# Kernel optimization log

Hardware: AMD Instinct MI355X
Metric: run time of the kernel (lower is better)

The kernel has to match this reference:

```python
import jax, jax.numpy as jnp
import numpy as np
from functools import partial

DN = ('NCHW', 'OIHW', 'NCHW')

def _conv(x, w, b, stride, pad):
    y = jax.lax.conv_general_dilated(x, w, (stride, stride), [(pad, pad), (pad, pad)], dimension_numbers=DN)
    return y + b[None, :, None, None]

def _leaky(x, s):
    return jnp.where(x >= 0, x, s * x)

def _lstm_gates(pre, c):
    # PyTorch gate order: i, f, g, o
    i, f, g, o = jnp.split(pre, 4, axis=-1)
    c_new = jax.nn.sigmoid(f) * c + jax.nn.sigmoid(i) * jnp.tanh(g)
    h_new = jax.nn.sigmoid(o) * jnp.tanh(c_new)
    return h_new, c_new

def setup_inputs() -> dict:
    key = jax.random.key(0)
    ks = iter(jax.random.split(key, 32))
    s = 0.05
    d = {}
    d['x'] = jax.random.normal(next(ks), (128, 3, 64, 64), jnp.float32)
    # conv stack params
    d['w1'] = jax.random.normal(next(ks), (64, 3, 7, 7)) * s;   d['b1'] = jnp.zeros((64,))
    d['w2'] = jax.random.normal(next(ks), (128, 64, 7, 7)) * s; d['b2'] = jnp.zeros((128,))
    d['w3'] = jax.random.normal(next(ks), (256, 128, 5, 5)) * s; d['b3'] = jnp.zeros((256,))
    d['w4'] = jax.random.normal(next(ks), (512, 256, 5, 5)) * s; d['b4'] = jnp.zeros((512,))
    d['w5'] = jax.random.normal(next(ks), (512, 512, 5, 5)) * s; d['b5'] = jnp.zeros((512,))
    # 2-layer LSTM (hidden=512), PyTorch layout: W_ih [4H, In], W_hh [4H, H]
    H = 512
    for l in range(2):
        d[f'wih{l}'] = jax.random.normal(next(ks), (4 * H, H)) * s
        d[f'whh{l}'] = jax.random.normal(next(ks), (4 * H, H)) * s
        d[f'bih{l}'] = jnp.zeros((4 * H,))
        d[f'bhh{l}'] = jnp.zeros((4 * H,))
    # FC head
    d['fw1'] = jax.random.normal(next(ks), (512, 512)) * s; d['fb1'] = jnp.zeros((512,))
    d['fw2'] = jax.random.normal(next(ks), (13, 512)) * s;  d['fb2'] = jnp.zeros((13,))
    return d

TIMESTEPS = 20

def reference(x, w1, b1, w2, b2, w3, b3, w4, b4, w5, b5,
              wih0, whh0, bih0, bhh0, wih1, whh1, bih1, bhh1,
              fw1, fb1, fw2, fb2):
    B = x.shape[0]
    h = _conv(x, w1, b1, 2, 3); h = _leaky(h, 0.2)
    h = _conv(h, w2, b2, 2, 0); h = _leaky(h, 0.2)
    h = _conv(h, w3, b3, 1, 0); h = _leaky(h, 0.2)
    h = _conv(h, w4, b4, 1, 0); h = _leaky(h, 0.2)
    h = _conv(h, w5, b5, 1, 0); h = _leaky(h, 0.2)
    feat = h.reshape(B, -1)  # [B, 512]
    H = 512
    # input to layer-0 is constant across timesteps: precompute Wx once
    xW0 = feat @ wih0.T + bih0 + bhh0  # [B, 4H]
    zeros = jnp.zeros((B, H), feat.dtype)

    def step(carry, _):
        h0, c0, h1, c1 = carry
        h0n, c0n = _lstm_gates(xW0 + h0 @ whh0.T, c0)
        pre1 = h0n @ wih1.T + bih1 + bhh1 + h1 @ whh1.T
        h1n, c1n = _lstm_gates(pre1, c1)
        return (h0n, c0n, h1n, c1n), h1n

    _, ys = jax.lax.scan(step, (zeros, zeros, zeros, zeros), None, length=TIMESTEPS)
    y = ys.reshape(TIMESTEPS * B, H)
    y = _leaky(y @ fw1.T + fb1, 0.01)
    y = jax.nn.sigmoid(y @ fw2.T + fb2)
    return y
```

## Files before the change

### kernel.cpp

```cpp
#include <hip/hip_runtime.h>
#include <math.h>

typedef _Float16 half_t;
typedef __attribute__((ext_vector_type(8))) _Float16 f16x8;
typedef __attribute__((ext_vector_type(4))) _Float16 f16x4;
typedef __attribute__((ext_vector_type(4))) float f32x4;

#define LEAKY(v, s) ((v) >= 0.f ? (v) : (s) * (v))

__device__ __forceinline__ float sig_(float x) { return 1.f / (1.f + expf(-x)); }
__device__ __forceinline__ half_t f2h(float f) { return (half_t)f; }

#define GLD(gp, lp)                                              \
  __builtin_amdgcn_global_load_lds(                              \
      (const __attribute__((address_space(1))) void*)(gp),       \
      (__attribute__((address_space(3))) void*)(lp), 16, 0, 0)

#define PHASE_WAIT(N)                                            \
  asm volatile("s_waitcnt vmcnt(" #N ")" ::: "memory");          \
  __builtin_amdgcn_s_barrier();                                  \
  __builtin_amdgcn_sched_barrier(0)

#define QOFF0 2048LL
#define QOFF1 4096LL
#define QOFF2 135168LL
#define QOFF3 266240LL
#define QOFF4 5283840LL
#define QOFF5 5310464LL
#define QOFF6 6359040LL
#define QOFF7 6621184LL
#define QOFF8 7669760LL
#define QOFF9 9766912LL

__global__ void prep_all(
    const float* __restrict__ x, const float* __restrict__ w1,
    const float* __restrict__ wih0, const float* __restrict__ whh0,
    const float* __restrict__ bih0, const float* __restrict__ bhh0,
    const float* __restrict__ wih1, const float* __restrict__ whh1,
    const float* __restrict__ bih1, const float* __restrict__ bhh1,
    const float* __restrict__ fw1,
    float* __restrict__ bg0, float* __restrict__ bg1,
    float* __restrict__ czero, unsigned* __restrict__ hzero,
    half_t* __restrict__ xpad, half_t* __restrict__ w1r,
    half_t* __restrict__ wih0h, half_t* __restrict__ fw1h,
    half_t* __restrict__ wcat0h, half_t* __restrict__ wcat1h) {
  long long i = (long long)blockIdx.x * blockDim.x + threadIdx.x;
  if (i < QOFF0) {
    bg0[i] = bih0[i] + bhh0[i];
  } else if (i < QOFF1) {
    long long j = i - QOFF0;
    bg1[j] = bih1[j] + bhh1[j];
  } else if (i < QOFF2) {
    czero[i - QOFF1] = 0.f;
  } else if (i < QOFF3) {
    hzero[i - QOFF2] = 0u;
  } else if (i < QOFF4) {
    long long j = i - QOFF3;
    int c = j & 7;
    long long t = j >> 3;
    int iw = t % 70; t /= 70;
    int ih = t % 70;
    int n = t / 70;
    float v = 0.f;
    if (c < 3 && ih >= 3 && ih < 67 && iw >= 3 && iw < 67)
      v = x[((n * 3 + c) * 64 + (ih - 3)) * 64 + (iw - 3)];
    xpad[j] = f2h(v);
  } else if (i < QOFF5) {
    int j = (int)(i - QOFF4);
    int kg = j % 416, co = j / 416;
    int ci = kg & 7, tap = kg >> 3;
    float v = 0.f;
    if (tap < 49 && ci < 3) {
      int kh = tap / 7, kw = tap % 7;
      v = w1[((co * 3 + ci) * 7 + kh) * 7 + kw];
    }
    w1r[j] = f2h(v);
  } else if (i < QOFF6) {
    int j = (int)(i - QOFF5);
    wih0h[j] = f2h(wih0[j]);
  } else if (i < QOFF7) {
    int j = (int)(i - QOFF6);
    fw1h[j] = f2h(fw1[j]);
  } else if (i < QOFF8) {
    int j = (int)(i - QOFF7);
    int r = j >> 9, k = j & 511;
    int u = r >> 2, g = r & 3;
    wcat0h[j] = f2h(whh0[(g * 512 + u) * 512 + k]);
  } else if (i < QOFF9) {
    int j = (int)(i - QOFF8);
    int r = j >> 10, k = j & 1023;
    int u = r >> 2, g = r & 3;
    int row = g * 512 + u;
    wcat1h[j] = f2h(k < 512 ? wih1[row * 512 + k] : whh1[row * 512 + (k - 512)]);
  }
}

__global__ __launch_bounds__(256) void prep_wT(
    const float* __restrict__ w2, const float* __restrict__ w3,
    const float* __restrict__ w4, const float* __restrict__ w5,
    half_t* __restrict__ w2r, half_t* __restrict__ w3r,
    half_t* __restrict__ w4r, half_t* __restrict__ w5r) {
  __shared__ float T[12800];
  int bid = blockIdx.x, tid = threadIdx.x;
  const float* W;
  half_t* D;
  int co, Cin, TAP, lg2;
  if (bid < 128) {
    W = w2; D = w2r; co = bid; Cin = 64; TAP = 49; lg2 = 6;
  } else if (bid < 384) {
    W = w3; D = w3r; co = bid - 128; Cin = 128; TAP = 25; lg2 = 7;
  } else if (bid < 896) {
    W = w4; D = w4r; co = bid - 384; Cin = 256; TAP = 25; lg2 = 8;
  } else {
    W = w5; D = w5r; co = bid - 896; Cin = 512; TAP = 25; lg2 = 9;
  }
  int n = Cin * TAP;
  const float* src = W + (size_t)co * n;
  for (int i = tid; i < n; i += 256) T[i] = src[i];
  __syncthreads();
  half_t* dst = D + (size_t)co * n;
  for (int j = tid; j < n; j += 256) {
    int ci = j & (Cin - 1);
    int tap = j >> lg2;
    dst[j] = f2h(T[ci * TAP + tap]);
  }
}

template <int KW, int S, int LOG2CIN, int OUTMODE>
__global__ __launch_bounds__(256) void conv_mfma(
    const half_t* __restrict__ xin, const half_t* __restrict__ wr,
    const float* __restrict__ bias, void* __restrict__ outp,
    int Hin, int Win, int Hout, int Wout, int Cout, int K, int ktiles, float slope,
    long long zstride) {
  constexpr int CIN = 1 << LOG2CIN;
  __shared__ half_t lds[4][4096];
  const int tid = threadIdx.x;
  const int lane = tid & 63, wid = tid >> 6;
  const int sRow = tid >> 2, sCh = tid & 3;
  const int sSwz = sCh ^ ((sRow ^ (sRow >> 2)) & 3);
  const int kt0 = blockIdx.z * ktiles;
  const half_t* gArow = wr + (size_t)(blockIdx.y * 64 + sRow) * K + sSwz * 8;
  int p = blockIdx.x * 64 + sRow;
  int hw = Hout * Wout;
  int n = p / hw;
  int rem = p - n * hw;
  int oh = rem / Wout;
  int ow = rem - oh * Wout;
  const half_t* xb = xin + ((size_t)(n * Hin + oh * S) * Win + ow * S) * CIN;
  const int fr = lane & 15, fc = lane >> 4;
  const int r0 = (wid & 1) * 32, c0 = (wid >> 1) * 32;
  const int sw = (fc ^ ((fr ^ (fr >> 2)) & 3)) * 8;
  const int ia0 = (r0 + fr) * 32 + sw;
  const int ia1 = (r0 + 16 + fr) * 32 + sw;
  const int ib0 = 2048 + (c0 + fr) * 32 + sw;
  const int ib1 = 2048 + (c0 + 16 + fr) * 32 + sw;

  auto stage = [&](int t, int buf) {
    GLD(gArow + (size_t)(kt0 + t) * 32, &lds[buf][wid * 512]);
    int kg = (kt0 + t) * 32 + sSwz * 8;
    int ci = kg & (CIN - 1);
    int tap = kg >> LOG2CIN;
    int kh = tap / KW, kw = tap - kh * KW;
    GLD(xb + (kh * Win + kw) * CIN + ci, &lds[buf][2048 + wid * 512]);
  };

  f32x4 acc00 = {0.f, 0.f, 0.f, 0.f};
  f32x4 acc01 = acc00, acc10 = acc00, acc11 = acc00;

  auto compute = [&](int buf) {
    const half_t* L = &lds[buf][0];
    f16x8 a0 = *(const f16x8*)&L[ia0];
    f16x8 a1 = *(const f16x8*)&L[ia1];
    f16x8 b0 = *(const f16x8*)&L[ib0];
    f16x8 b1 = *(const f16x8*)&L[ib1];
    acc00 = __builtin_amdgcn_mfma_f32_16x16x32_f16(a0, b0, acc00, 0, 0, 0);
    acc01 = __builtin_amdgcn_mfma_f32_16x16x32_f16(a0, b1, acc01, 0, 0, 0);
    acc10 = __builtin_amdgcn_mfma_f32_16x16x32_f16(a1, b0, acc10, 0, 0, 0);
    acc11 = __builtin_amdgcn_mfma_f32_16x16x32_f16(a1, b1, acc11, 0, 0, 0);
  };

  stage(0, 0);
  stage(1, 1);
  stage(2, 2);
  int t = 0;
  for (; t < ktiles - 3; ++t) {
    PHASE_WAIT(4);
    stage(t + 3, (t + 3) & 3);
    compute(t & 3);
  }
  PHASE_WAIT(4);
  compute(t & 3);
  ++t;
  PHASE_WAIT(2);
  compute(t & 3);
  ++t;
  PHASE_WAIT(0);
  compute(t & 3);

#pragma unroll
  for (int am = 0; am < 2; ++am) {
#pragma unroll
    for (int bn = 0; bn < 2; ++bn) {
      f32x4 a = am == 0 ? (bn == 0 ? acc00 : acc01) : (bn == 0 ? acc10 : acc11);
      int co = blockIdx.y * 64 + r0 + am * 16 + fc * 4;
      int px = blockIdx.x * 64 + c0 + bn * 16 + fr;
      size_t o = (size_t)px * Cout + co;
      if (OUTMODE == 2) {
        float* pb = (float*)outp + (size_t)blockIdx.z * zstride;
        *(f32x4*)&pb[o] = a;
      } else {
        f32x4 bb = *(const f32x4*)&bias[co];
        f32x4 v;
#pragma unroll
        for (int j = 0; j < 4; ++j) {
          float tt = a[j] + bb[j];
          v[j] = LEAKY(tt, slope);
        }
        if (OUTMODE == 1) {
          *(f32x4*)&((float*)outp)[o] = v;
        } else {
          f16x4 hv;
#pragma unroll
          for (int j = 0; j < 4; ++j) hv[j] = f2h(v[j]);
          *(f16x4*)&((half_t*)outp)[o] = hv;
        }
      }
    }
  }
}

template <int KW, int S, int LOG2CIN, int OUTMODE>
__global__ __launch_bounds__(256) void conv_mfma128(
    const half_t* __restrict__ xin, const half_t* __restrict__ wr,
    const float* __restrict__ bias, void* __restrict__ outp,
    int Hin, int Win, int Hout, int Wout, int Cout, int K, int ktiles, float slope,
    long long zstride) {
  constexpr int CIN = 1 << LOG2CIN;
  __shared__ half_t lds[4][8192];
  const int tid = threadIdx.x;
  const int lane = tid & 63, wid = tid >> 6;
  const int sRow = tid >> 2, sCh = tid & 3;
  const int sSwz = sCh ^ ((sRow ^ (sRow >> 2)) & 3);
  const int kt0 = blockIdx.z * ktiles;
  const half_t* gA0 = wr + (size_t)(blockIdx.y * 128 + sRow) * K + sSwz * 8;
  const half_t* gA1 = wr + (size_t)(blockIdx.y * 128 + 64 + sRow) * K + sSwz * 8;
  int hw = Hout * Wout;
  int p0 = blockIdx.x * 128 + sRow;
  int n0 = p0 / hw, r0p = p0 - n0 * hw, oh0 = r0p / Wout, ow0 = r0p - oh0 * Wout;
  const half_t* xb0 = xin + ((size_t)(n0 * Hin + oh0 * S) * Win + ow0 * S) * CIN;
  int p1 = p0 + 64;
  int n1 = p1 / hw, r1p = p1 - n1 * hw, oh1 = r1p / Wout, ow1 = r1p - oh1 * Wout;
  const half_t* xb1 = xin + ((size_t)(n1 * Hin + oh1 * S) * Win + ow1 * S) * CIN;

  const int fr = lane & 15, fc = lane >> 4;
  const int wr_ = wid & 1, wc_ = wid >> 1;
  const int sw = (fc ^ ((fr ^ (fr >> 2)) & 3)) * 8;
  const int iaB = (wr_ * 64 + fr) * 32 + sw;
  const int ibB = 4096 + (wc_ * 64 + fr) * 32 + sw;

  auto stage = [&](int t, int buf) {
    half_t* LB = &lds[buf][0];
    GLD(gA0 + (size_t)(kt0 + t) * 32, LB + wid * 512);
    GLD(gA1 + (size_t)(kt0 + t) * 32, LB + 2048 + wid * 512);
    int kg = (kt0 + t) * 32 + sSwz * 8;
    int ci = kg & (CIN - 1);
    int tap = kg >> LOG2CIN;
    int kh = tap / KW, kw = tap - kh * KW;
    int xoff = (kh * Win + kw) * CIN + ci;
    GLD(xb0 + xoff, LB + 4096 + wid * 512);
    GLD(xb1 + xoff, LB + 6144 + wid * 512);
  };

  f32x4 acc[4][4];
#pragma unroll
  for (int i = 0; i < 4; ++i)
#pragma unroll
    for (int j = 0; j < 4; ++j) acc[i][j] = (f32x4){0.f, 0.f, 0.f, 0.f};

  auto compute = [&](int buf) {
    const half_t* L = &lds[buf][0];
    f16x8 a[4], b[4];
#pragma unroll
    for (int fi = 0; fi < 4; ++fi) a[fi] = *(const f16x8*)&L[iaB + fi * 512];
#pragma unroll
    for (int fj = 0; fj < 4; ++fj) b[fj] = *(const f16x8*)&L[ibB + fj * 512];
#pragma unroll
    for (int fi = 0; fi < 4; ++fi)
#pragma unroll
      for (int fj = 0; fj < 4; ++fj)
        acc[fi][fj] = __builtin_amdgcn_mfma_f32_16x16x32_f16(a[fi], b[fj], acc[fi][fj], 0, 0, 0);
  };

  stage(0, 0);
  stage(1, 1);
  stage(2, 2);
  int t = 0;
  for (; t < ktiles - 3; ++t) {
    PHASE_WAIT(8);
    stage(t + 3, (t + 3) & 3);
    compute(t & 3);
  }
  PHASE_WAIT(8);
  compute(t & 3);
  ++t;
  PHASE_WAIT(4);
  compute(t & 3);
  ++t;
  PHASE_WAIT(0);
  compute(t & 3);

#pragma unroll
  for (int fi = 0; fi < 4; ++fi) {
#pragma unroll
    for (int fj = 0; fj < 4; ++fj) {
      int co = blockIdx.y * 128 + wr_ * 64 + fi * 16 + fc * 4;
      int px = blockIdx.x * 128 + wc_ * 64 + fj * 16 + fr;
      size_t o = (size_t)px * Cout + co;
      if (OUTMODE == 2) {
        float* pb = (float*)outp + (size_t)blockIdx.z * zstride;
        *(f32x4*)&pb[o] = acc[fi][fj];
      } else {
        f32x4 bb = *(const f32x4*)&bias[co];
        f16x4 hv;
#pragma unroll
        for (int j = 0; j < 4; ++j) {
          float tt = acc[fi][fj][j] + bb[j];
          hv[j] = f2h(LEAKY(tt, slope));
        }
        *(f16x4*)&((half_t*)outp)[o] = hv;
      }
    }
  }
}

__global__ void finalize_part(const float* __restrict__ pb, const float* __restrict__ bias,
                              half_t* __restrict__ out, int size, int nz) {
  int i = blockIdx.x * blockDim.x + threadIdx.x;
  if (i >= size) return;
  float s = bias[i & 511];
  for (int z = 0; z < nz; ++z) s += pb[(size_t)z * size + i];
  out[i] = f2h(LEAKY(s, 0.2f));
}

__global__ __launch_bounds__(256) void lstm_fused(
    const half_t* __restrict__ h0in, half_t* __restrict__ h0out,
    const half_t* __restrict__ h1in, half_t* __restrict__ h1out,
    const half_t* __restrict__ wcat0, const half_t* __restrict__ wcat1,
    const float* __restrict__ xw0, const float* __restrict__ bg1,
    float* __restrict__ c0, float* __restrict__ c1,
    half_t* __restrict__ ysout, int roles) {
  const bool isL1 = (roles == 2) || (blockIdx.z == 1);
  const int NT = isL1 ? 16 : 8;
  const half_t* wcat = isL1 ? wcat1 : wcat0;
  float* c = isL1 ? c1 : c0;
  half_t* hout = isL1 ? h1out : h0out;
  const int K = NT * 64;

  __shared__ half_t lds[4][8192];
  const int tid = threadIdx.x;
  const int lane = tid & 63, wid = tid >> 6;
  const int ybase = blockIdx.y * 64, bbase = blockIdx.x * 64;
  const int rA0 = wid * 16 + (lane >> 3);
  const int rA1 = rA0 + 8;
  const int chS = ((lane & 7) ^ ((lane >> 3) & 7)) * 8;
  const half_t* gA0 = wcat + (size_t)(ybase + rA0) * K + chS;
  const half_t* gA1 = wcat + (size_t)(ybase + rA1) * K + chS;
  const size_t hb0 = (size_t)(bbase + rA0) * 512 + chS;
  const size_t hb1 = (size_t)(bbase + rA1) * 512 + chS;

  auto stage = [&](int t, int buf) {
    GLD(gA0 + t * 64, &lds[buf][wid * 1024]);
    GLD(gA1 + t * 64, &lds[buf][wid * 1024 + 512]);
    const half_t* hs = (isL1 && t >= 8) ? h1in : h0in;
    int koff = (isL1 && t >= 8) ? (t - 8) * 64 : t * 64;
    GLD(hs + hb0 + koff, &lds[buf][4096 + wid * 1024]);
    GLD(hs + hb1 + koff, &lds[buf][4096 + wid * 1024 + 512]);
  };

  const int fr = lane & 15, fc = lane >> 4;
  const int wr_ = wid & 1, wc_ = wid >> 1;

  f32x4 acc[2][2];
#pragma unroll
  for (int fi = 0; fi < 2; ++fi)
#pragma unroll
    for (int fj = 0; fj < 2; ++fj) acc[fi][fj] = (f32x4){0.f, 0.f, 0.f, 0.f};

  auto compute = [&](int buf) {
    const half_t* L = &lds[buf][0];
#pragma unroll
    for (int s = 0; s < 2; ++s) {
      f16x8 a[2], b[2];
#pragma unroll
      for (int fi = 0; fi < 2; ++fi) {
        int row = wr_ * 32 + fi * 16 + fr;
        a[fi] = *(const f16x8*)&L[row * 64 + (((s * 4 + fc) ^ (fr & 7)) * 8)];
      }
#pragma unroll
      for (int fj = 0; fj < 2; ++fj) {
        int brow = wc_ * 32 + fj * 16 + fr;
        b[fj] = *(const f16x8*)&L[4096 + brow * 64 + (((s * 4 + fc) ^ (fr & 7)) * 8)];
      }
#pragma unroll
      for (int fi = 0; fi < 2; ++fi)
#pragma unroll
        for (int fj = 0; fj < 2; ++fj)
          acc[fi][fj] = __builtin_amdgcn_mfma_f32_16x16x32_f16(a[fi], b[fj], acc[fi][fj], 0, 0, 0);
    }
  };

  stage(0, 0);
  stage(1, 1);
  stage(2, 2);
  int t = 0;
  for (; t < NT - 3; ++t) {
    PHASE_WAIT(8);
    stage(t + 3, (t + 3) & 3);
    compute(t & 3);
  }
  PHASE_WAIT(8);
  compute(t & 3);
  ++t;
  PHASE_WAIT(4);
  compute(t & 3);
  ++t;
  PHASE_WAIT(0);
  compute(t & 3);

#pragma unroll
  for (int fi = 0; fi < 2; ++fi) {
#pragma unroll
    for (int fj = 0; fj < 2; ++fj) {
      int Rb = ybase + wr_ * 32 + fi * 16 + fc * 4;
      int u = Rb >> 2;
      int b = bbase + wc_ * 32 + fj * 16 + fr;
      float p[4];
#pragma unroll
      for (int j = 0; j < 4; ++j) {
        float s = acc[fi][fj][j];
        s += isL1 ? bg1[j * 512 + u] : xw0[b * 2048 + j * 512 + u];
        p[j] = s;
      }
      int ci = b * 512 + u;
      float cprev = c[ci];
      float ig = sig_(p[0]);
      float fg = sig_(p[1]);
      float gg = tanhf(p[2]);
      float og = sig_(p[3]);
      float cn = fg * cprev + ig * gg;
      float hn = og * tanhf(cn);
      c[ci] = cn;
      hout[ci] = f2h(hn);
      if (isL1) ysout[ci] = f2h(hn);
    }
  }
}

__global__ void fc2_sigmoid(const half_t* __restrict__ in, const float* __restrict__ w,
                            const float* __restrict__ b, float* __restrict__ out) {
  int idx = blockIdx.x * blockDim.x + threadIdx.x;
  if (idx >= 2560 * 13) return;
  int j = idx % 13, r = idx / 13;
  const half_t* ip = in + (size_t)r * 512;
  const float* wp = w + j * 512;
  float s = b[j];
  for (int k = 0; k < 512; k += 8) {
    f16x8 hv = *(const f16x8*)&ip[k];
#pragma unroll
    for (int q = 0; q < 8; ++q) s = fmaf((float)hv[q], wp[k + q], s);
  }
  out[idx] = sig_(s);
}

extern "C" void kernel_launch(void* const* d_in, const int* in_sizes, int n_in,
                              void* d_out, int out_size, void* d_ws, size_t ws_size,
                              hipStream_t stream) {
  const float* x   = (const float*)d_in[0];
  const float* w1  = (const float*)d_in[1];  const float* b1 = (const float*)d_in[2];
  const float* w2  = (const float*)d_in[3];  const float* b2 = (const float*)d_in[4];
  const float* w3  = (const float*)d_in[5];  const float* b3 = (const float*)d_in[6];
  const float* w4  = (const float*)d_in[7];  const float* b4 = (const float*)d_in[8];
  const float* w5  = (const float*)d_in[9];  const float* b5 = (const float*)d_in[10];
  const float* wih0 = (const float*)d_in[11]; const float* whh0 = (const float*)d_in[12];
  const float* bih0 = (const float*)d_in[13]; const float* bhh0 = (const float*)d_in[14];
  const float* wih1 = (const float*)d_in[15]; const float* whh1 = (const float*)d_in[16];
  const float* bih1 = (const float*)d_in[17]; const float* bhh1 = (const float*)d_in[18];
  const float* fw1 = (const float*)d_in[19]; const float* fb1 = (const float*)d_in[20];
  const float* fw2 = (const float*)d_in[21]; const float* fb2 = (const float*)d_in[22];
  float* out = (float*)d_out;

  float* bg0 = (float*)d_ws;
  float* bg1 = bg0 + 2048;
  float* xw0 = bg1 + 2048;
  float* c0  = xw0 + 262144;
  float* c1  = c0 + 65536;
  half_t* h0a = (half_t*)(c1 + 65536);
  half_t* h0b = h0a + 65536;
  half_t* h1a = h0b + 65536;
  half_t* h1b = h1a + 65536;
  half_t* BUF1 = h1b + 65536;
  half_t* BUF2 = BUF1 + 8388608;
  half_t* w1r  = BUF2 + 2768896;
  half_t* w2r  = w1r + 26624;
  half_t* w3r  = w2r + 401408;
  half_t* w4r  = w3r + 819200;
  half_t* w5r  = w4r + 3276800;
  half_t* wih0h  = w5r + 6553600;
  half_t* wcat0h = wih0h + 1048576;
  half_t* wcat1h = wcat0h + 1048576;
  half_t* fw1h   = wcat1h + 2097152;
  half_t* xpad   = fw1h + 262144;
  float* pbC = (float*)xpad;

  half_t* A1 = BUF1;
  half_t* A2 = BUF2;
  half_t* A3 = BUF1;
  half_t* A4 = BUF2;
  half_t* feat = BUF1;
  half_t* ys   = BUF2;
  half_t* fc1o = BUF2 + 1310720;

  dim3 blk(256);

  prep_all<<<38152, blk, 0, stream>>>(
      x, w1, wih0, whh0, bih0, bhh0, wih1, whh1, bih1, bhh1, fw1,
      bg0, bg1, c0, (unsigned*)h0a, xpad, w1r, wih0h, fw1h, wcat0h, wcat1h);
  prep_wT<<<1408, blk, 0, stream>>>(w2, w3, w4, w5, w2r, w3r, w4r, w5r);

  conv_mfma<7, 2, 3, 0><<<dim3(2048, 1, 1), blk, 0, stream>>>(
      xpad, w1r, b1, A1, 70, 70, 32, 32, 64, 416, 13, 0.2f, 0);
  conv_mfma128<7, 2, 6, 0><<<dim3(169, 1, 1), blk, 0, stream>>>(
      A1, w2r, b2, A2, 32, 32, 13, 13, 128, 3136, 98, 0.2f, 0);
  conv_mfma128<5, 1, 7, 0><<<dim3(81, 2, 1), blk, 0, stream>>>(
      A2, w3r, b3, A3, 13, 13, 9, 9, 256, 3200, 100, 0.2f, 0);
  conv_mfma128<5, 1, 8, 2><<<dim3(25, 4, 2), blk, 0, stream>>>(
      A3, w4r, b4, pbC, 9, 9, 5, 5, 512, 6400, 100, 0.2f, (long long)3200 * 512);
  finalize_part<<<6400, blk, 0, stream>>>(pbC, b4, A4, 1638400, 2);
  conv_mfma<5, 1, 9, 2><<<dim3(2, 8, 25), blk, 0, stream>>>(
      A4, w5r, b5, pbC, 5, 5, 1, 1, 512, 12800, 16, 0.2f, (long long)65536);
  finalize_part<<<256, blk, 0, stream>>>(pbC, b5, feat, 65536, 25);

  conv_mfma<1, 1, 9, 1><<<dim3(2, 32, 1), blk, 0, stream>>>(
      feat, wih0h, bg0, xw0, 1, 1, 1, 1, 2048, 512, 16, 1.0f, 0);

  half_t* h0buf[2] = {h0a, h0b};
  half_t* h1buf[2] = {h1a, h1b};
  lstm_fused<<<dim3(2, 32, 1), blk, 0, stream>>>(
      h0a, h0b, h1a, h1a, wcat0h, wcat1h, xw0, bg1, c0, c1, ys, 1);
  for (int t = 2; t <= 20; ++t) {
    lstm_fused<<<dim3(2, 32, 2), blk, 0, stream>>>(
        h0buf[(t - 1) & 1], h0buf[t & 1], h1buf[t & 1], h1buf[(t - 1) & 1],
        wcat0h, wcat1h, xw0, bg1, c0, c1, ys + (size_t)(t - 2) * 65536, 3);
  }
  lstm_fused<<<dim3(2, 32, 1), blk, 0, stream>>>(
      h0buf[0], h0buf[1], h1buf[1], h1buf[0],
      wcat0h, wcat1h, xw0, bg1, c0, c1, ys + (size_t)19 * 65536, 2);

  conv_mfma<1, 1, 9, 0><<<dim3(40, 8, 1), blk, 0, stream>>>(
      ys, fw1h, fb1, fc1o, 1, 1, 1, 1, 512, 512, 16, 0.01f, 0);
  fc2_sigmoid<<<130, blk, 0, stream>>>(fc1o, fw2, fb2, out);
}
```

Measured before the change: 411.8 us.

## Split-K conv2-conv4 with fp16 partials and 1D grid tile ordering

Conv layers 2, 3 and 4 now use split-K (2, 2 and 4 K-splits) so more workgroups are launched on an under-filled GPU (169, 162 and 200 blocks before). Each split writes its partial sums as fp16, and a new vectorised finalize_h kernel adds the partials, the bias and the leaky ReLU. The grid is flattened to 1D, with the y/z indices innermost so that neighbouring blocks share the same input pixels. This costs extra kernel launches and partial-sum traffic. Rounding the partials to fp16 also loses some precision.

```diff
diff --git a/kernel.cpp b/kernel.cpp
--- a/kernel.cpp
+++ b/kernel.cpp
@@ -234,18 +234,23 @@
     const half_t* __restrict__ xin, const half_t* __restrict__ wr,
     const float* __restrict__ bias, void* __restrict__ outp,
     int Hin, int Win, int Hout, int Wout, int Cout, int K, int ktiles, float slope,
-    long long zstride) {
+    long long zstride, int Y, int G) {
   constexpr int CIN = 1 << LOG2CIN;
   __shared__ half_t lds[4][8192];
+  const int L = blockIdx.x;
+  const int bx = L / G;
+  const int g = L % G;
+  const int by = g % Y;
+  const int bz = g / Y;
   const int tid = threadIdx.x;
   const int lane = tid & 63, wid = tid >> 6;
   const int sRow = tid >> 2, sCh = tid & 3;
   const int sSwz = sCh ^ ((sRow ^ (sRow >> 2)) & 3);
-  const int kt0 = blockIdx.z * ktiles;
-  const half_t* gA0 = wr + (size_t)(blockIdx.y * 128 + sRow) * K + sSwz * 8;
-  const half_t* gA1 = wr + (size_t)(blockIdx.y * 128 + 64 + sRow) * K + sSwz * 8;
+  const int kt0 = bz * ktiles;
+  const half_t* gA0 = wr + (size_t)(by * 128 + sRow) * K + sSwz * 8;
+  const half_t* gA1 = wr + (size_t)(by * 128 + 64 + sRow) * K + sSwz * 8;
   int hw = Hout * Wout;
-  int p0 = blockIdx.x * 128 + sRow;
+  int p0 = bx * 128 + sRow;
   int n0 = p0 / hw, r0p = p0 - n0 * hw, oh0 = r0p / Wout, ow0 = r0p - oh0 * Wout;
   const half_t* xb0 = xin + ((size_t)(n0 * Hin + oh0 * S) * Win + ow0 * S) * CIN;
   int p1 = p0 + 64;
@@ -278,12 +283,12 @@
     for (int j = 0; j < 4; ++j) acc[i][j] = (f32x4){0.f, 0.f, 0.f, 0.f};
 
   auto compute = [&](int buf) {
-    const half_t* L = &lds[buf][0];
+    const half_t* L2 = &lds[buf][0];
     f16x8 a[4], b[4];
 #pragma unroll
-    for (int fi = 0; fi < 4; ++fi) a[fi] = *(const f16x8*)&L[iaB + fi * 512];
-#pragma unroll
-    for (int fj = 0; fj < 4; ++fj) b[fj] = *(const f16x8*)&L[ibB + fj * 512];
+    for (int fi = 0; fi < 4; ++fi) a[fi] = *(const f16x8*)&L2[iaB + fi * 512];
+#pragma unroll
+    for (int fj = 0; fj < 4; ++fj) b[fj] = *(const f16x8*)&L2[ibB + fj * 512];
 #pragma unroll
     for (int fi = 0; fi < 4; ++fi)
 #pragma unroll
@@ -313,12 +318,15 @@
   for (int fi = 0; fi < 4; ++fi) {
 #pragma unroll
     for (int fj = 0; fj < 4; ++fj) {
-      int co = blockIdx.y * 128 + wr_ * 64 + fi * 16 + fc * 4;
-      int px = blockIdx.x * 128 + wc_ * 64 + fj * 16 + fr;
+      int co = by * 128 + wr_ * 64 + fi * 16 + fc * 4;
+      int px = bx * 128 + wc_ * 64 + fj * 16 + fr;
       size_t o = (size_t)px * Cout + co;
-      if (OUTMODE == 2) {
-        float* pb = (float*)outp + (size_t)blockIdx.z * zstride;
-        *(f32x4*)&pb[o] = acc[fi][fj];
+      if (OUTMODE == 3) {
+        half_t* pb = (half_t*)outp + (size_t)bz * zstride;
+        f16x4 hv;
+#pragma unroll
+        for (int j = 0; j < 4; ++j) hv[j] = f2h(acc[fi][fj][j]);
+        *(f16x4*)&pb[o] = hv;
       } else {
         f32x4 bb = *(const f32x4*)&bias[co];
         f16x4 hv;
@@ -340,6 +348,26 @@
   float s = bias[i & 511];
   for (int z = 0; z < nz; ++z) s += pb[(size_t)z * size + i];
   out[i] = f2h(LEAKY(s, 0.2f));
+}
+
+__global__ void finalize_h(const half_t* __restrict__ pb, const float* __restrict__ bias,
+                           half_t* __restrict__ out, int size8, int nz, int cmask,
+                           long long zstride) {
+  int idx = blockIdx.x * blockDim.x + threadIdx.x;
+  if (idx >= size8) return;
+  long long i = (long long)idx * 8;
+  float s[8];
+#pragma unroll
+  for (int q = 0; q < 8; ++q) s[q] = bias[(int)((i + q) & cmask)];
+  for (int z = 0; z < nz; ++z) {
+    f16x8 v = *(const f16x8*)&pb[(size_t)z * zstride + i];
+#pragma unroll
+    for (int q = 0; q < 8; ++q) s[q] += (float)v[q];
+  }
+  f16x8 o;
+#pragma unroll
+  for (int q = 0; q < 8; ++q) o[q] = f2h(LEAKY(s[q], 0.2f));
+  *(f16x8*)&out[i] = o;
 }
 
 __global__ __launch_bounds__(256) void lstm_fused(
@@ -510,6 +538,7 @@
   half_t* wcat1h = wcat0h + 1048576;
   half_t* fw1h   = wcat1h + 2097152;
   half_t* xpad   = fw1h + 262144;
+  half_t* pbH = xpad;
   float* pbC = (float*)xpad;
 
   half_t* A1 = BUF1;
@@ -529,13 +558,15 @@
 
   conv_mfma<7, 2, 3, 0><<<dim3(2048, 1, 1), blk, 0, stream>>>(
       xpad, w1r, b1, A1, 70, 70, 32, 32, 64, 416, 13, 0.2f, 0);
-  conv_mfma128<7, 2, 6, 0><<<dim3(169, 1, 1), blk, 0, stream>>>(
-      A1, w2r, b2, A2, 32, 32, 13, 13, 128, 3136, 98, 0.2f, 0);
-  conv_mfma128<5, 1, 7, 0><<<dim3(81, 2, 1), blk, 0, stream>>>(
-      A2, w3r, b3, A3, 13, 13, 9, 9, 256, 3200, 100, 0.2f, 0);
-  conv_mfma128<5, 1, 8, 2><<<dim3(25, 4, 2), blk, 0, stream>>>(
-      A3, w4r, b4, pbC, 9, 9, 5, 5, 512, 6400, 100, 0.2f, (long long)3200 * 512);
-  finalize_part<<<6400, blk, 0, stream>>>(pbC, b4, A4, 1638400, 2);
+  conv_mfma128<7, 2, 6, 3><<<338, blk, 0, stream>>>(
+      A1, w2r, b2, pbH, 32, 32, 13, 13, 128, 3136, 49, 0.2f, 2768896LL, 1, 2);
+  finalize_h<<<1352, blk, 0, stream>>>(pbH, b2, A2, 346112, 2, 127, 2768896LL);
+  conv_mfma128<5, 1, 7, 3><<<324, blk, 0, stream>>>(
+      A2, w3r, b3, pbH, 13, 13, 9, 9, 256, 3200, 50, 0.2f, 2654208LL, 2, 4);
+  finalize_h<<<1296, blk, 0, stream>>>(pbH, b3, A3, 331776, 2, 255, 2654208LL);
+  conv_mfma128<5, 1, 8, 3><<<400, blk, 0, stream>>>(
+      A3, w4r, b4, pbH, 9, 9, 5, 5, 512, 6400, 50, 0.2f, 1638400LL, 4, 16);
+  finalize_h<<<800, blk, 0, stream>>>(pbH, b4, A4, 204800, 4, 511, 1638400LL);
   conv_mfma<5, 1, 9, 2><<<dim3(2, 8, 25), blk, 0, stream>>>(
       A4, w5r, b5, pbC, 5, 5, 1, 1, 512, 12800, 16, 0.2f, (long long)65536);
   finalize_part<<<256, blk, 0, stream>>>(pbC, b5, feat, 65536, 25);
```

New measurement: 399.7 us. 2.9% less time.
